# Kernel optimization log

Hardware: AMD Instinct MI355X
Metric: run time of the kernel (lower is better)

## Reference

```python
import jax, jax.numpy as jnp
import numpy as np

B, N, F_DIM = 64, 4096, 64
K_SLOTS, D, N_ITERS = 8, 64, 3
EPS = 1e-8
LN_EPS = 1e-5  # torch LayerNorm default


def layernorm(x, g, b):
    mu = jnp.mean(x, axis=-1, keepdims=True)
    var = jnp.mean(jnp.square(x - mu), axis=-1, keepdims=True)
    return (x - mu) * jax.lax.rsqrt(var + LN_EPS) * g + b


def gru_cell(x, h, w_ih, w_hh, b_ih, b_hh):
    # torch.nn.GRUCell semantics; weights are [3D, D] with gate order r, z, n
    gi = x @ w_ih.T + b_ih
    gh = h @ w_hh.T + b_hh
    i_r, i_z, i_n = jnp.split(gi, 3, axis=-1)
    h_r, h_z, h_n = jnp.split(gh, 3, axis=-1)
    r = jax.nn.sigmoid(i_r + h_r)
    z = jax.nn.sigmoid(i_z + h_z)
    n = jnp.tanh(i_n + r * h_n)
    return (1.0 - z) * n + z * h


def setup_inputs() -> dict:
    key = jax.random.key(0)
    ks = jax.random.split(key, 16)
    f32 = jnp.float32
    s = 0.05  # small init scale for weights
    return {
        "inputs": jax.random.normal(ks[0], (B, N, F_DIM), f32),
        "slots_noise": jax.random.normal(ks[1], (B, K_SLOTS, D), f32),
        "slots_mu": jax.random.normal(ks[2], (1, 1, D), f32) * s,
        "slots_log_sigma": jax.random.normal(ks[3], (1, 1, D), f32) * s,
        "Wq": jax.random.normal(ks[4], (D, D), f32) * s,
        "Wk": jax.random.normal(ks[5], (D, F_DIM), f32) * s,
        "Wv": jax.random.normal(ks[6], (D, F_DIM), f32) * s,
        "gru_w_ih": jax.random.normal(ks[7], (3 * D, D), f32) * s,
        "gru_w_hh": jax.random.normal(ks[8], (3 * D, D), f32) * s,
        "gru_b_ih": jnp.zeros((3 * D,), f32),
        "gru_b_hh": jnp.zeros((3 * D,), f32),
        "mlp_w1": jax.random.normal(ks[9], (2 * D, D), f32) * s,
        "mlp_b1": jnp.zeros((2 * D,), f32),
        "mlp_w2": jax.random.normal(ks[10], (D, 2 * D), f32) * s,
        "mlp_b2": jnp.zeros((D,), f32),
        "ln_in_g": jnp.ones((F_DIM,), f32), "ln_in_b": jnp.zeros((F_DIM,), f32),
        "ln_slots_g": jnp.ones((D,), f32), "ln_slots_b": jnp.zeros((D,), f32),
        "ln_mlp_g": jnp.ones((D,), f32), "ln_mlp_b": jnp.zeros((D,), f32),
    }


def reference(inputs, slots_noise, slots_mu, slots_log_sigma, Wq, Wk, Wv,
              gru_w_ih, gru_w_hh, gru_b_ih, gru_b_hh,
              mlp_w1, mlp_b1, mlp_w2, mlp_b2,
              ln_in_g, ln_in_b, ln_slots_g, ln_slots_b, ln_mlp_g, ln_mlp_b):
    x = layernorm(inputs, ln_in_g, ln_in_b)          # [B, N, F]
    k = jnp.einsum('bnf,df->bnd', x, Wk)             # [B, N, D]
    v = jnp.einsum('bnf,df->bnd', x, Wv)             # [B, N, D]

    slots = slots_mu + jnp.exp(slots_log_sigma) * slots_noise  # [B, K, D]
    scale = D ** -0.5

    for _ in range(N_ITERS):
        slots_prev = slots
        s_n = layernorm(slots, ln_slots_g, ln_slots_b)
        q = jnp.einsum('bkd,ed->bke', s_n, Wq)                  # [B, K, D]
        attn_logits = jnp.einsum('bnd,bkd->bnk', k, q) * scale  # [B, N, K]
        attn = jax.nn.softmax(attn_logits, axis=-1) + EPS       # softmax over slots
        attn = attn / jnp.sum(attn, axis=1, keepdims=True)      # renormalize over N
        updates = jnp.einsum('bnk,bnd->bkd', attn, v)           # [B, K, D]
        slots = gru_cell(updates.reshape(-1, D), slots_prev.reshape(-1, D),
                         gru_w_ih, gru_w_hh, gru_b_ih, gru_b_hh).reshape(B, K_SLOTS, D)
        h = layernorm(slots, ln_mlp_g, ln_mlp_b)
        h = jax.nn.relu(h @ mlp_w1.T + mlp_b1) @ mlp_w2.T + mlp_b2
        slots = slots + h
    return slots
```

## Files before the change

### kernel.cpp

```cpp
#include <hip/hip_runtime.h>
#include <math.h>

#define NN 4096
#define LN_EPS 1e-5f
#define EPS 1e-8f

typedef unsigned short ushortT;
typedef unsigned int uintT;
typedef __attribute__((ext_vector_type(8))) short short8;
typedef __attribute__((ext_vector_type(4))) float f32x4;
typedef __attribute__((ext_vector_type(2))) float f32x2;
typedef __attribute__((ext_vector_type(4))) unsigned short us4;

#define OFF_XN    0L
#define OFF_QU    8388608L
#define OFF_AP    8486912L
#define OFF_CP    9273344L
#define OFF_SLOTS 9285632L
#define OFF_WIHT  9383936L
#define OFF_WHHT  9396224L
#define OFF_W1T   9408512L
#define OFF_W2T   9416704L
#define OFF_WQT   9424896L
#define OFF_WVT   9428992L
#define OFF_CNT   9433088L
#define OFF_RDY   9433280L

__device__ __forceinline__ float wredsum(float v) {
#pragma unroll
  for (int off = 32; off > 0; off >>= 1) v += __shfl_xor(v, off);
  return v;
}

__device__ __forceinline__ ushortT f2bf(float f) {
  uintT b = __float_as_uint(f);
  b += 0x7fff + ((b >> 16) & 1);
  return (ushortT)(b >> 16);
}

__device__ __forceinline__ uintT pack2bf(float lo, float hi) {
  return (uintT)f2bf(lo) | ((uintT)f2bf(hi) << 16);
}

__device__ __forceinline__ void store2_coh(float* p, f32x2 v) {
  asm volatile("global_store_dwordx2 %0, %1, off sc0 sc1" :: "v"(p), "v"(v) : "memory");
}
__device__ __forceinline__ void store1f_coh(float* p, float v) {
  asm volatile("global_store_dword %0, %1, off sc0 sc1" :: "v"(p), "v"(v) : "memory");
}
__device__ __forceinline__ void store1u_coh(uintT* p, uintT v) {
  asm volatile("global_store_dword %0, %1, off sc0 sc1" :: "v"(p), "v"(v) : "memory");
}
__device__ __forceinline__ uintT load1u_coh(const uintT* p) {
  uintT r;
  asm volatile("global_load_dword %0, %1, off sc0 sc1\n\t"
               "s_waitcnt vmcnt(0)" : "=v"(r) : "v"(p) : "memory");
  return r;
}
__device__ __forceinline__ void drain_vm() {
  asm volatile("s_waitcnt vmcnt(0)" ::: "memory");
}

__global__ __launch_bounds__(256) void k_prep(
    const float* __restrict__ w_ih, const float* __restrict__ w_hh,
    const float* __restrict__ w1, const float* __restrict__ w2,
    const float* __restrict__ Wq, const float* __restrict__ Wv,
    float* __restrict__ wihT, float* __restrict__ whhT,
    float* __restrict__ w1T, float* __restrict__ w2T, float* __restrict__ wqT,
    float* __restrict__ wvT, uintT* __restrict__ cnt, uintT* __restrict__ ready)
{
  int idx = blockIdx.x * 256 + threadIdx.x;
  if (idx < 12288) {
    int j = idx >> 6, f = idx & 63;
    wihT[f * 192 + j] = w_ih[idx];
  } else if (idx < 24576) {
    int i = idx - 12288; int j = i >> 6, f = i & 63;
    whhT[f * 192 + j] = w_hh[i];
  } else if (idx < 32768) {
    int i = idx - 24576; int j = i >> 6, f = i & 63;
    w1T[f * 128 + j] = w1[i];
  } else if (idx < 40960) {
    int i = idx - 32768; int d = i >> 7, j = i & 127;
    w2T[j * 64 + d] = w2[i];
  } else if (idx < 45056) {
    int i = idx - 40960; int e = i >> 6, d = i & 63;
    wqT[d * 64 + e] = Wq[i];
  } else if (idx < 49152) {
    int i = idx - 45056; int d = i >> 6, f = i & 63;
    wvT[f * 64 + d] = Wv[i];
  } else if (idx < 49344) {
    cnt[idx - 49152] = 0u;
  } else if (idx < 49408) {
    ready[idx - 49344] = 0u;
  }
}

__global__ __launch_bounds__(256) void k_ln_init(
    const float* __restrict__ inp,
    const float* __restrict__ g, const float* __restrict__ bbv,
    ushortT* __restrict__ xnG,
    const float* __restrict__ noise, const float* __restrict__ smu,
    const float* __restrict__ slsig, const float* __restrict__ wqT,
    const float* __restrict__ Wk,
    const float* __restrict__ g_sl, const float* __restrict__ b_sl,
    float* __restrict__ slotsV, uintT* __restrict__ qU)
{
  __shared__ __align__(16) ushortT xnF[4096];
  const int tid = threadIdx.x;
  const int lane = tid & 63;
  const int wave = tid >> 6;

  if (blockIdx.x >= 4096) {
    const int bi = blockIdx.x - 4096;
    const int row = bi * 4 + wave;
    const int b = row >> 3, ks = row & 7;
    float* SI = (float*)&xnF[0];
    float* Sw = SI + (wave << 9);

    float s0 = fmaf(expf(slsig[lane]), noise[row * 64 + lane], smu[lane]);
    slotsV[row * 64 + lane] = s0;

    float mu = wredsum(s0) * (1.f / 64.f);
    float dx = s0 - mu;
    float var = wredsum(dx * dx) * (1.f / 64.f);
    float sn = dx * rsqrtf(var + LN_EPS) * g_sl[lane] + b_sl[lane];
    Sw[lane] = sn;
    float qe = 0.f;
#pragma unroll 16
    for (int d = 0; d < 64; ++d) qe = fmaf(Sw[d], wqT[d * 64 + lane], qe);
    Sw[64 + lane] = qe;
    float qp = 0.f;
#pragma unroll 16
    for (int e = 0; e < 64; ++e) qp = fmaf(Sw[64 + e], Wk[e * 64 + lane], qp);
    Sw[128 + lane] = qp * 0.125f;
    if (lane < 32) {
      const int kb = lane >> 4, lrow = (lane >> 2) & 3, j2 = lane & 3;
      const int fA = kb * 32 + lrow * 8 + 2 * j2;
      uintT u = pack2bf(Sw[128 + fA], Sw[128 + fA + 1]);
      qU[((b * 2 + kb) * 64 + lrow * 16 + ks) * 4 + j2] = u;
#pragma unroll
      for (int v = 0; v < 3; ++v)
        qU[v * 32768 + ((b * 2 + kb) * 64 + lrow * 16 + 8 + ks) * 4 + j2] = 0u;
    }
    return;
  }

  const int l15 = lane & 15, q = lane >> 4;
  const int tile = blockIdx.x;
  const int b = tile >> 6;
  const int c = tile & 63;
  const int n0 = c << 6;
  const float* rowbase = inp + (((long)b * NN + n0) << 6);
  const float4 g4 = *(const float4*)&g[l15 << 2];
  const float4 b4 = *(const float4*)&bbv[l15 << 2];

#pragma unroll
  for (int i = 0; i < 4; ++i) {
    const int row = (wave << 4) + (i << 2) + q;
    float4 x = *(const float4*)&rowbase[(row << 6) + (l15 << 2)];
    float s = x.x + x.y + x.z + x.w;
    s += __shfl_xor(s, 1); s += __shfl_xor(s, 2);
    s += __shfl_xor(s, 4); s += __shfl_xor(s, 8);
    const float mu = s * (1.f / 64.f);
    float4 dx = {x.x - mu, x.y - mu, x.z - mu, x.w - mu};
    float ss = dx.x * dx.x + dx.y * dx.y + dx.z * dx.z + dx.w * dx.w;
    ss += __shfl_xor(ss, 1); ss += __shfl_xor(ss, 2);
    ss += __shfl_xor(ss, 4); ss += __shfl_xor(ss, 8);
    const float rs = rsqrtf(ss * (1.f / 64.f) + LN_EPS);
    us4 p = {f2bf(dx.x * rs * g4.x + b4.x), f2bf(dx.y * rs * g4.y + b4.y),
             f2bf(dx.z * rs * g4.z + b4.z), f2bf(dx.w * rs * g4.w + b4.w)};
    *(us4*)&xnF[((((wave << 1) + (l15 >> 3)) << 6) + (((l15 & 7) >> 1) << 4)
                 + (row & 15)) * 8 + ((l15 & 1) << 2)] = p;
  }
  __syncthreads();

  ushortT* dst = xnG + ((long)(b * 64 + c) << 12);
  short8 v0 = *(const short8*)&xnF[tid << 4];
  short8 v1 = *(const short8*)&xnF[(tid << 4) + 8];
  *(short8*)&dst[tid << 4] = v0;
  *(short8*)&dst[(tid << 4) + 8] = v1;
}

__global__ __launch_bounds__(256, 2) void k_attn(
    const ushortT* __restrict__ xnG, uintT* __restrict__ qU,
    float* __restrict__ accPart, float* __restrict__ colPart,
    uintT* __restrict__ cnt, uintT* __restrict__ ready,
    float* __restrict__ slotsV,
    const float* __restrict__ wihT, const float* __restrict__ whhT,
    const float* __restrict__ w1T, const float* __restrict__ w2T,
    const float* __restrict__ wqT, const float* __restrict__ Wk,
    const float* __restrict__ wvT,
    const float* __restrict__ b_ih, const float* __restrict__ b_hh,
    const float* __restrict__ mb1, const float* __restrict__ mb2,
    const float* __restrict__ g_ml, const float* __restrict__ b_ml,
    const float* __restrict__ g_sl, const float* __restrict__ b_sl,
    float* __restrict__ dout)
{
  __shared__ __align__(16) ushortT XW[4][4096];
  __shared__ int lastFlag;
  const int tid = threadIdx.x;
  const int lane = tid & 63;
  const int wave = tid >> 6;
  const int l15 = lane & 15, q = lane >> 4;
  const int b = blockIdx.x >> 3;
  const int e = blockIdx.x & 7;

  ushortT* xT = &XW[wave][0];

  const ushortT* pc0 = xnG + ((long)(b * 64 + (e << 3) + wave) << 12);
  const ushortT* pc1 = pc0 + (4L << 12);

  short8 kA0[4][2], kA1[4][2];
#pragma unroll
  for (int mt = 0; mt < 4; ++mt)
#pragma unroll
    for (int kb = 0; kb < 2; ++kb) {
      kA0[mt][kb] = *(const short8*)&pc0[((mt * 2 + kb) * 64 + lane) << 3];
      kA1[mt][kb] = *(const short8*)&pc1[((mt * 2 + kb) * 64 + lane) << 3];
    }

  short8 vB0[4][2], vB1[4][2];
  {
    const int h = ((lane >> 5) << 2) | (((lane & 15) >> 3) << 1) | ((lane >> 4) & 1);
    const int jp = lane & 7;
    const int lpA = (((lane >> 4) & 1) << 3) + (((lane & 15) >> 3) << 4);
#pragma unroll
    for (int ch = 0; ch < 2; ++ch) {
#pragma unroll
      for (int mt = 0; mt < 4; ++mt)
#pragma unroll
        for (int kb = 0; kb < 2; ++kb) {
          const int fb = (kb * 4 + ((lane >> 5) << 1) + (mt >> 1)) << 9;
          const int lm = lpA + ((mt & 1) << 5);
          const short8 src8 = ch ? kA1[mt][kb] : kA0[mt][kb];
          const ushortT* src = (const ushortT*)&src8;
#pragma unroll
          for (int j = 0; j < 8; ++j)
            xT[fb + (((lm + j) ^ h) << 3) + jp] = src[j];
        }
#pragma unroll
      for (int nt = 0; nt < 4; ++nt)
#pragma unroll
        for (int ks = 0; ks < 2; ++ks) {
          const int frag = nt * 2 + ks;
          const int hr = ((nt & 1) << 2) | (((lane >> 4) & 1) << 1) | ((lane >> 3) & 1);
          short8 v = *(const short8*)&xT[(frag << 9) + ((lane ^ hr) << 3)];
          if (ch) vB1[nt][ks] = v; else vB0[nt][ks] = v;
        }
    }
  }

  for (int it = 0; it < 3; ++it) {
    if (it > 0) {
      if (tid == 0) {
        while (load1u_coh(&ready[b]) < (uintT)it) __builtin_amdgcn_s_sleep(2);
      }
      __syncthreads();
    }

    const uintT* qIt = qU + it * 32768;
    short8 qB[2];
#pragma unroll
    for (int kb = 0; kb < 2; ++kb)
      qB[kb] = *(const short8*)&qIt[((b * 2 + kb) * 64 + lane) * 4];

    f32x4 accP[4];
#pragma unroll
    for (int nt = 0; nt < 4; ++nt) accP[nt] = (f32x4){0.f, 0.f, 0.f, 0.f};
    float csum = 0.f;

#pragma unroll
    for (int ch = 0; ch < 2; ++ch) {
      f32x4 accL[4];
#pragma unroll
      for (int mt = 0; mt < 4; ++mt) {
        const short8 a0 = ch ? kA1[mt][0] : kA0[mt][0];
        const short8 a1 = ch ? kA1[mt][1] : kA0[mt][1];
        accL[mt] = (f32x4){0.f, 0.f, 0.f, 0.f};
        accL[mt] = __builtin_amdgcn_mfma_f32_16x16x32_bf16(a0, qB[0], accL[mt], 0, 0, 0);
        accL[mt] = __builtin_amdgcn_mfma_f32_16x16x32_bf16(a1, qB[1], accL[mt], 0, 0, 0);
      }

      ushortT* attnF = &XW[wave][0];
#pragma unroll
      for (int mt = 0; mt < 4; ++mt) {
        float av[4];
#pragma unroll
        for (int r = 0; r < 4; ++r) {
          float lv = accL[mt][r];
          float mx = lv;
          mx = fmaxf(mx, __shfl_xor(mx, 1));
          mx = fmaxf(mx, __shfl_xor(mx, 2));
          mx = fmaxf(mx, __shfl_xor(mx, 4));
          float ev = __expf(lv - mx);
          float sv = ev;
          sv += __shfl_xor(sv, 1); sv += __shfl_xor(sv, 2); sv += __shfl_xor(sv, 4);
          float a = ev * (1.f / sv) + EPS;
          av[r] = a;
          csum += a;
        }
        us4 p = {f2bf(av[0]), f2bf(av[1]), f2bf(av[2]), f2bf(av[3])};
        *(us4*)&attnF[((((mt >> 1) << 6) + (((mt & 1) * 2 + (q >> 1)) << 4)
                        + l15) << 3) + ((q & 1) << 2)] = p;
      }

      short8 pA0 = *(const short8*)&attnF[(0 * 64 + lane) << 3];
      short8 pA1 = *(const short8*)&attnF[(1 * 64 + lane) << 3];

#pragma unroll
      for (int nt = 0; nt < 4; ++nt) {
        const short8 v0 = ch ? vB1[nt][0] : vB0[nt][0];
        const short8 v1 = ch ? vB1[nt][1] : vB0[nt][1];
        accP[nt] = __builtin_amdgcn_mfma_f32_16x16x32_bf16(pA0, v0, accP[nt], 0, 0, 0);
        accP[nt] = __builtin_amdgcn_mfma_f32_16x16x32_bf16(pA1, v1, accP[nt], 0, 0, 0);
      }
    }

    csum += __shfl_xor(csum, 16);
    csum += __shfl_xor(csum, 32);

    float* accLw = (float*)&XW[wave][1024];
    float* colLw = (float*)&XW[wave][2048];
    if (q < 2) {
#pragma unroll
      for (int nt = 0; nt < 4; ++nt)
#pragma unroll
        for (int r = 0; r < 4; ++r)
          accLw[(q * 4 + r) * 64 + nt * 16 + l15] = accP[nt][r];
    }
    if (q == 0 && l15 < 8) colLw[l15] = csum;
    __syncthreads();

    float* apIt = accPart + ((long)(it * 64 + b) * 8 + e) * 512;
    float* cpIt = colPart + ((long)(it * 64 + b) * 8 + e) * 8;
    {
      const int o = tid * 2;
      f32x2 s;
#pragma unroll
      for (int r = 0; r < 2; ++r) {
        const int oo = o + r;
        s[r] = *((float*)&XW[0][1024] + oo) + *((float*)&XW[1][1024] + oo)
             + *((float*)&XW[2][1024] + oo) + *((float*)&XW[3][1024] + oo);
      }
      store2_coh(&apIt[o], s);
    }
    if (tid < 8) {
      float s = *((float*)&XW[0][2048] + tid) + *((float*)&XW[1][2048] + tid)
              + *((float*)&XW[2][2048] + tid) + *((float*)&XW[3][2048] + tid);
      store1f_coh(&cpIt[tid], s);
    }

    drain_vm();
    __syncthreads();
    if (tid == 0) lastFlag = (atomicAdd(&cnt[it * 64 + b], 1u) == 7u);
    __syncthreads();

    if (lastFlag) {
      const int ks0 = wave, ks1 = wave + 4;
      const int row0 = b * 8 + ks0, row1 = b * 8 + ks1;
      const float* apB = accPart + (long)(it * 64 + b) * 8 * 512;
      const float* cpB = colPart + (long)(it * 64 + b) * 8 * 8;
      const float* slIt = slotsV + it * 32768;

      float csv0 = 0.f, csv1 = 0.f, t0 = 0.f, t1 = 0.f;
#pragma unroll
      for (int ee = 0; ee < 8; ++ee) {
        csv0 += cpB[ee * 8 + ks0];
        csv1 += cpB[ee * 8 + ks1];
        t0 += apB[ee * 512 + ks0 * 64 + lane];
        t1 += apB[ee * 512 + ks1 * 64 + lane];
      }
      t0 /= csv0; t1 /= csv1;
      const float h0 = slIt[row0 * 64 + lane];
      const float h1 = slIt[row1 * 64 + lane];

      float* S = (float*)&XW[wave][0];

      S[256 + lane] = t0; S[320 + lane] = t1;
      float u0 = 0.f, u1 = 0.f;
#pragma unroll 4
      for (int f = 0; f < 64; ++f) {
        const float wv = wvT[f * 64 + lane];
        u0 = fmaf(S[256 + f], wv, u0);
        u1 = fmaf(S[320 + f], wv, u1);
      }

      S[lane] = u0; S[64 + lane] = u1; S[128 + lane] = h0; S[192 + lane] = h1;

      float gir0 = b_ih[lane], giz0 = b_ih[64 + lane], gin0 = b_ih[128 + lane];
      float ghr0 = b_hh[lane], ghz0 = b_hh[64 + lane], ghn0 = b_hh[128 + lane];
      float gir1 = gir0, giz1 = giz0, gin1 = gin0;
      float ghr1 = ghr0, ghz1 = ghz0, ghn1 = ghn0;
#pragma unroll 4
      for (int f = 0; f < 64; ++f) {
        const float wr = wihT[f * 192 + lane], wz = wihT[f * 192 + 64 + lane],
                    wn = wihT[f * 192 + 128 + lane];
        const float vr = whhT[f * 192 + lane], vz = whhT[f * 192 + 64 + lane],
                    vn = whhT[f * 192 + 128 + lane];
        const float a0 = S[f], a1 = S[64 + f], c0 = S[128 + f], c1 = S[192 + f];
        gir0 = fmaf(a0, wr, gir0); gir1 = fmaf(a1, wr, gir1);
        giz0 = fmaf(a0, wz, giz0); giz1 = fmaf(a1, wz, giz1);
        gin0 = fmaf(a0, wn, gin0); gin1 = fmaf(a1, wn, gin1);
        ghr0 = fmaf(c0, vr, ghr0); ghr1 = fmaf(c1, vr, ghr1);
        ghz0 = fmaf(c0, vz, ghz0); ghz1 = fmaf(c1, vz, ghz1);
        ghn0 = fmaf(c0, vn, ghn0); ghn1 = fmaf(c1, vn, ghn1);
      }
      const float r0 = 1.f / (1.f + expf(-(gir0 + ghr0)));
      const float z0 = 1.f / (1.f + expf(-(giz0 + ghz0)));
      const float n0 = tanhf(fmaf(r0, ghn0, gin0));
      const float hn0 = (1.f - z0) * n0 + z0 * h0;
      const float r1 = 1.f / (1.f + expf(-(gir1 + ghr1)));
      const float z1 = 1.f / (1.f + expf(-(giz1 + ghz1)));
      const float n1 = tanhf(fmaf(r1, ghn1, gin1));
      const float hn1 = (1.f - z1) * n1 + z1 * h1;

      float mu0 = wredsum(hn0) * (1.f / 64.f);
      float dx0 = hn0 - mu0;
      float va0 = wredsum(dx0 * dx0) * (1.f / 64.f);
      const float ln0 = dx0 * rsqrtf(va0 + LN_EPS) * g_ml[lane] + b_ml[lane];
      float mu1 = wredsum(hn1) * (1.f / 64.f);
      float dx1 = hn1 - mu1;
      float va1 = wredsum(dx1 * dx1) * (1.f / 64.f);
      const float ln1 = dx1 * rsqrtf(va1 + LN_EPS) * g_ml[lane] + b_ml[lane];
      S[256 + lane] = ln0; S[320 + lane] = ln1;

      float h1a0 = mb1[lane], h1b0 = mb1[64 + lane];
      float h1a1 = h1a0, h1b1 = h1b0;
#pragma unroll 4
      for (int f = 0; f < 64; ++f) {
        const float wa = w1T[f * 128 + lane], wb = w1T[f * 128 + 64 + lane];
        const float l0 = S[256 + f], l1 = S[320 + f];
        h1a0 = fmaf(l0, wa, h1a0); h1a1 = fmaf(l1, wa, h1a1);
        h1b0 = fmaf(l0, wb, h1b0); h1b1 = fmaf(l1, wb, h1b1);
      }
      h1a0 = fmaxf(h1a0, 0.f); h1b0 = fmaxf(h1b0, 0.f);
      h1a1 = fmaxf(h1a1, 0.f); h1b1 = fmaxf(h1b1, 0.f);
      S[lane] = h1a0; S[64 + lane] = h1b0;
      S[128 + lane] = h1a1; S[192 + lane] = h1b1;

      float o0 = mb2[lane], o1 = mb2[lane];
#pragma unroll 4
      for (int j = 0; j < 128; ++j) {
        const float w2v = w2T[j * 64 + lane];
        o0 = fmaf(S[j], w2v, o0);
        o1 = fmaf(S[128 + j], w2v, o1);
      }
      const float sn0 = hn0 + o0;
      const float sn1 = hn1 + o1;

      if (it == 2) {
        dout[row0 * 64 + lane] = sn0;
        dout[row1 * 64 + lane] = sn1;
      } else {
        float* slN = slotsV + (it + 1) * 32768;
        store1f_coh(&slN[row0 * 64 + lane], sn0);
        store1f_coh(&slN[row1 * 64 + lane], sn1);

        float m20 = wredsum(sn0) * (1.f / 64.f);
        float d20 = sn0 - m20;
        float v20 = wredsum(d20 * d20) * (1.f / 64.f);
        const float sq0 = d20 * rsqrtf(v20 + LN_EPS) * g_sl[lane] + b_sl[lane];
        float m21 = wredsum(sn1) * (1.f / 64.f);
        float d21 = sn1 - m21;
        float v21 = wredsum(d21 * d21) * (1.f / 64.f);
        const float sq1 = d21 * rsqrtf(v21 + LN_EPS) * g_sl[lane] + b_sl[lane];
        S[256 + lane] = sq0; S[320 + lane] = sq1;
        float qe0 = 0.f, qe1 = 0.f;
#pragma unroll 8
        for (int d = 0; d < 64; ++d) {
          const float wq = wqT[d * 64 + lane];
          qe0 = fmaf(S[256 + d], wq, qe0);
          qe1 = fmaf(S[320 + d], wq, qe1);
        }
        S[256 + lane] = qe0; S[320 + lane] = qe1;
        float qp0 = 0.f, qp1 = 0.f;
#pragma unroll 8
        for (int e2 = 0; e2 < 64; ++e2) {
          const float wk = Wk[e2 * 64 + lane];
          qp0 = fmaf(S[256 + e2], wk, qp0);
          qp1 = fmaf(S[320 + e2], wk, qp1);
        }
        S[384 + lane] = qp0 * 0.125f;
        S[448 + lane] = qp1 * 0.125f;
        {
          uintT* qN = qU + (it + 1) * 32768;
          const int rr = lane >> 5, L5 = lane & 31;
          const int kb = L5 >> 4, lrow = (L5 >> 2) & 3, j2 = L5 & 3;
          const int fA = kb * 32 + lrow * 8 + 2 * j2;
          const int ksr = rr ? ks1 : ks0;
          uintT u = pack2bf(S[384 + rr * 64 + fA], S[384 + rr * 64 + fA + 1]);
          store1u_coh(&qN[((b * 2 + kb) * 64 + lrow * 16 + ksr) * 4 + j2], u);
        }
        drain_vm();
        __syncthreads();
        if (tid == 0) atomicAdd(&ready[b], 1u);
      }
    }
  }
}

extern "C" void kernel_launch(void* const* d_in, const int* in_sizes, int n_in,
                              void* d_out, int out_size, void* d_ws, size_t ws_size,
                              hipStream_t stream) {
  const float* inp   = (const float*)d_in[0];
  const float* noise = (const float*)d_in[1];
  const float* smu   = (const float*)d_in[2];
  const float* slsig = (const float*)d_in[3];
  const float* Wq    = (const float*)d_in[4];
  const float* Wk    = (const float*)d_in[5];
  const float* Wv    = (const float*)d_in[6];
  const float* w_ih  = (const float*)d_in[7];
  const float* w_hh  = (const float*)d_in[8];
  const float* b_ih  = (const float*)d_in[9];
  const float* b_hh  = (const float*)d_in[10];
  const float* w1    = (const float*)d_in[11];
  const float* b1    = (const float*)d_in[12];
  const float* w2    = (const float*)d_in[13];
  const float* b2    = (const float*)d_in[14];
  const float* g_in  = (const float*)d_in[15];
  const float* bi_in = (const float*)d_in[16];
  const float* g_sl  = (const float*)d_in[17];
  const float* bi_sl = (const float*)d_in[18];
  const float* g_ml  = (const float*)d_in[19];
  const float* bi_ml = (const float*)d_in[20];

  float* ws      = (float*)d_ws;
  ushortT* xnG   = (ushortT*)(ws + OFF_XN);
  uintT* qU      = (uintT*)(ws + OFF_QU);
  float* ap      = ws + OFF_AP;
  float* cp      = ws + OFF_CP;
  float* sl      = ws + OFF_SLOTS;
  float* wihT    = ws + OFF_WIHT;
  float* whhT    = ws + OFF_WHHT;
  float* w1T     = ws + OFF_W1T;
  float* w2T     = ws + OFF_W2T;
  float* wqT     = ws + OFF_WQT;
  float* wvT     = ws + OFF_WVT;
  uintT* cnt     = (uintT*)(ws + OFF_CNT);
  uintT* rdy     = (uintT*)(ws + OFF_RDY);

  k_prep<<<194, 256, 0, stream>>>(w_ih, w_hh, w1, w2, Wq, Wv,
                                  wihT, whhT, w1T, w2T, wqT, wvT, cnt, rdy);
  k_ln_init<<<4224, 256, 0, stream>>>(inp, g_in, bi_in, xnG,
                                      noise, smu, slsig, wqT, Wk, g_sl, bi_sl,
                                      sl, qU);
  k_attn<<<512, 256, 0, stream>>>(xnG, qU, ap, cp, cnt, rdy, sl,
                                  wihT, whhT, w1T, w2T, wqT, Wk, wvT,
                                  b_ih, b_hh, b1, b2, g_ml, bi_ml, g_sl, bi_sl,
                                  (float*)d_out);
}
```

Measured before the change: 268.4 us.

## Fuse input LayerNorm into attention kernel and drop bf16 staging buffer

Input LayerNorm and bf16 conversion now run inside the persistent attention kernel, reading the fp32 inputs directly instead of a 16 MB bf16 intermediate written by a separate kernel. Slot init and q-projection move into the weight-prep kernel, which removes one launch. The V-operand transpose is recomputed through LDS on every iteration instead of being held in registers, which lowers register pressure but adds LDS traffic inside the loop. The trade-off is that the attention kernel reads 64 MB of fp32 instead of 32 MB of bf16, in return for skipping a write and a read of the intermediate.

```diff
diff --git a/kernel.cpp b/kernel.cpp
--- a/kernel.cpp
+++ b/kernel.cpp
@@ -12,19 +12,18 @@
 typedef __attribute__((ext_vector_type(2))) float f32x2;
 typedef __attribute__((ext_vector_type(4))) unsigned short us4;
 
-#define OFF_XN    0L
-#define OFF_QU    8388608L
-#define OFF_AP    8486912L
-#define OFF_CP    9273344L
-#define OFF_SLOTS 9285632L
-#define OFF_WIHT  9383936L
-#define OFF_WHHT  9396224L
-#define OFF_W1T   9408512L
-#define OFF_W2T   9416704L
-#define OFF_WQT   9424896L
-#define OFF_WVT   9428992L
-#define OFF_CNT   9433088L
-#define OFF_RDY   9433280L
+#define OFF_QU    0L
+#define OFF_AP    98304L
+#define OFF_CP    884736L
+#define OFF_SLOTS 897024L
+#define OFF_WIHT  995328L
+#define OFF_WHHT  1007616L
+#define OFF_W1T   1019904L
+#define OFF_W2T   1028096L
+#define OFF_WQT   1036288L
+#define OFF_WVT   1040384L
+#define OFF_CNT   1044480L
+#define OFF_RDY   1044672L
 
 __device__ __forceinline__ float wredsum(float v) {
 #pragma unroll
@@ -60,16 +59,61 @@
 __device__ __forceinline__ void drain_vm() {
   asm volatile("s_waitcnt vmcnt(0)" ::: "memory");
 }
+__device__ __forceinline__ void wait_lds() {
+  asm volatile("s_waitcnt lgkmcnt(0)" ::: "memory");
+}
 
 __global__ __launch_bounds__(256) void k_prep(
     const float* __restrict__ w_ih, const float* __restrict__ w_hh,
     const float* __restrict__ w1, const float* __restrict__ w2,
     const float* __restrict__ Wq, const float* __restrict__ Wv,
+    const float* __restrict__ Wk,
+    const float* __restrict__ noise, const float* __restrict__ smu,
+    const float* __restrict__ slsig,
+    const float* __restrict__ g_sl, const float* __restrict__ b_sl,
     float* __restrict__ wihT, float* __restrict__ whhT,
     float* __restrict__ w1T, float* __restrict__ w2T, float* __restrict__ wqT,
-    float* __restrict__ wvT, uintT* __restrict__ cnt, uintT* __restrict__ ready)
+    float* __restrict__ wvT, float* __restrict__ slotsV, uintT* __restrict__ qU,
+    uintT* __restrict__ cnt, uintT* __restrict__ ready)
 {
-  int idx = blockIdx.x * 256 + threadIdx.x;
+  const int tid = threadIdx.x;
+  if (blockIdx.x >= 194) {
+    __shared__ float SI[4][192];
+    const int lane = tid & 63, wave = tid >> 6;
+    const int bi = blockIdx.x - 194;
+    const int row = bi * 4 + wave;
+    const int b = row >> 3, ks = row & 7;
+    float* Sw = SI[wave];
+
+    float s0 = fmaf(expf(slsig[lane]), noise[row * 64 + lane], smu[lane]);
+    slotsV[row * 64 + lane] = s0;
+
+    float mu = wredsum(s0) * (1.f / 64.f);
+    float dx = s0 - mu;
+    float var = wredsum(dx * dx) * (1.f / 64.f);
+    float sn = dx * rsqrtf(var + LN_EPS) * g_sl[lane] + b_sl[lane];
+    Sw[lane] = sn;
+    float qe = 0.f;
+#pragma unroll 16
+    for (int d = 0; d < 64; ++d) qe = fmaf(Sw[d], Wq[lane * 64 + d], qe);
+    Sw[64 + lane] = qe;
+    float qp = 0.f;
+#pragma unroll 16
+    for (int e = 0; e < 64; ++e) qp = fmaf(Sw[64 + e], Wk[e * 64 + lane], qp);
+    Sw[128 + lane] = qp * 0.125f;
+    if (lane < 32) {
+      const int kb = lane >> 4, lrow = (lane >> 2) & 3, j2 = lane & 3;
+      const int fA = kb * 32 + lrow * 8 + 2 * j2;
+      uintT u = pack2bf(Sw[128 + fA], Sw[128 + fA + 1]);
+      qU[((b * 2 + kb) * 64 + lrow * 16 + ks) * 4 + j2] = u;
+#pragma unroll
+      for (int v = 0; v < 3; ++v)
+        qU[v * 32768 + ((b * 2 + kb) * 64 + lrow * 16 + 8 + ks) * 4 + j2] = 0u;
+    }
+    return;
+  }
+
+  int idx = blockIdx.x * 256 + tid;
   if (idx < 12288) {
     int j = idx >> 6, f = idx & 63;
     wihT[f * 192 + j] = w_ih[idx];
@@ -95,94 +139,10 @@
   }
 }
 
-__global__ __launch_bounds__(256) void k_ln_init(
+__global__ __launch_bounds__(256, 2) void k_attn(
     const float* __restrict__ inp,
-    const float* __restrict__ g, const float* __restrict__ bbv,
-    ushortT* __restrict__ xnG,
-    const float* __restrict__ noise, const float* __restrict__ smu,
-    const float* __restrict__ slsig, const float* __restrict__ wqT,
-    const float* __restrict__ Wk,
-    const float* __restrict__ g_sl, const float* __restrict__ b_sl,
-    float* __restrict__ slotsV, uintT* __restrict__ qU)
-{
-  __shared__ __align__(16) ushortT xnF[4096];
-  const int tid = threadIdx.x;
-  const int lane = tid & 63;
-  const int wave = tid >> 6;
-
-  if (blockIdx.x >= 4096) {
-    const int bi = blockIdx.x - 4096;
-    const int row = bi * 4 + wave;
-    const int b = row >> 3, ks = row & 7;
-    float* SI = (float*)&xnF[0];
-    float* Sw = SI + (wave << 9);
-
-    float s0 = fmaf(expf(slsig[lane]), noise[row * 64 + lane], smu[lane]);
-    slotsV[row * 64 + lane] = s0;
-
-    float mu = wredsum(s0) * (1.f / 64.f);
-    float dx = s0 - mu;
-    float var = wredsum(dx * dx) * (1.f / 64.f);
-    float sn = dx * rsqrtf(var + LN_EPS) * g_sl[lane] + b_sl[lane];
-    Sw[lane] = sn;
-    float qe = 0.f;
-#pragma unroll 16
-    for (int d = 0; d < 64; ++d) qe = fmaf(Sw[d], wqT[d * 64 + lane], qe);
-    Sw[64 + lane] = qe;
-    float qp = 0.f;
-#pragma unroll 16
-    for (int e = 0; e < 64; ++e) qp = fmaf(Sw[64 + e], Wk[e * 64 + lane], qp);
-    Sw[128 + lane] = qp * 0.125f;
-    if (lane < 32) {
-      const int kb = lane >> 4, lrow = (lane >> 2) & 3, j2 = lane & 3;
-      const int fA = kb * 32 + lrow * 8 + 2 * j2;
-      uintT u = pack2bf(Sw[128 + fA], Sw[128 + fA + 1]);
-      qU[((b * 2 + kb) * 64 + lrow * 16 + ks) * 4 + j2] = u;
-#pragma unroll
-      for (int v = 0; v < 3; ++v)
-        qU[v * 32768 + ((b * 2 + kb) * 64 + lrow * 16 + 8 + ks) * 4 + j2] = 0u;
-    }
-    return;
-  }
-
-  const int l15 = lane & 15, q = lane >> 4;
-  const int tile = blockIdx.x;
-  const int b = tile >> 6;
-  const int c = tile & 63;
-  const int n0 = c << 6;
-  const float* rowbase = inp + (((long)b * NN + n0) << 6);
-  const float4 g4 = *(const float4*)&g[l15 << 2];
-  const float4 b4 = *(const float4*)&bbv[l15 << 2];
-
-#pragma unroll
-  for (int i = 0; i < 4; ++i) {
-    const int row = (wave << 4) + (i << 2) + q;
-    float4 x = *(const float4*)&rowbase[(row << 6) + (l15 << 2)];
-    float s = x.x + x.y + x.z + x.w;
-    s += __shfl_xor(s, 1); s += __shfl_xor(s, 2);
-    s += __shfl_xor(s, 4); s += __shfl_xor(s, 8);
-    const float mu = s * (1.f / 64.f);
-    float4 dx = {x.x - mu, x.y - mu, x.z - mu, x.w - mu};
-    float ss = dx.x * dx.x + dx.y * dx.y + dx.z * dx.z + dx.w * dx.w;
-    ss += __shfl_xor(ss, 1); ss += __shfl_xor(ss, 2);
-    ss += __shfl_xor(ss, 4); ss += __shfl_xor(ss, 8);
-    const float rs = rsqrtf(ss * (1.f / 64.f) + LN_EPS);
-    us4 p = {f2bf(dx.x * rs * g4.x + b4.x), f2bf(dx.y * rs * g4.y + b4.y),
-             f2bf(dx.z * rs * g4.z + b4.z), f2bf(dx.w * rs * g4.w + b4.w)};
-    *(us4*)&xnF[((((wave << 1) + (l15 >> 3)) << 6) + (((l15 & 7) >> 1) << 4)
-                 + (row & 15)) * 8 + ((l15 & 1) << 2)] = p;
-  }
-  __syncthreads();
-
-  ushortT* dst = xnG + ((long)(b * 64 + c) << 12);
-  short8 v0 = *(const short8*)&xnF[tid << 4];
-  short8 v1 = *(const short8*)&xnF[(tid << 4) + 8];
-  *(short8*)&dst[tid << 4] = v0;
-  *(short8*)&dst[(tid << 4) + 8] = v1;
-}
-
-__global__ __launch_bounds__(256, 2) void k_attn(
-    const ushortT* __restrict__ xnG, uintT* __restrict__ qU,
+    const float* __restrict__ g_in, const float* __restrict__ b_in,
+    uintT* __restrict__ qU,
     float* __restrict__ accPart, float* __restrict__ colPart,
     uintT* __restrict__ cnt, uintT* __restrict__ ready,
     float* __restrict__ slotsV,
@@ -207,46 +167,42 @@
 
   ushortT* xT = &XW[wave][0];
 
-  const ushortT* pc0 = xnG + ((long)(b * 64 + (e << 3) + wave) << 12);
-  const ushortT* pc1 = pc0 + (4L << 12);
-
   short8 kA0[4][2], kA1[4][2];
-#pragma unroll
-  for (int mt = 0; mt < 4; ++mt)
-#pragma unroll
-    for (int kb = 0; kb < 2; ++kb) {
-      kA0[mt][kb] = *(const short8*)&pc0[((mt * 2 + kb) * 64 + lane) << 3];
-      kA1[mt][kb] = *(const short8*)&pc1[((mt * 2 + kb) * 64 + lane) << 3];
-    }
-
-  short8 vB0[4][2], vB1[4][2];
   {
-    const int h = ((lane >> 5) << 2) | (((lane & 15) >> 3) << 1) | ((lane >> 4) & 1);
-    const int jp = lane & 7;
-    const int lpA = (((lane >> 4) & 1) << 3) + (((lane & 15) >> 3) << 4);
+    const float4 g4 = *(const float4*)&g_in[l15 << 2];
+    const float4 b4 = *(const float4*)&b_in[l15 << 2];
 #pragma unroll
     for (int ch = 0; ch < 2; ++ch) {
+      const int chunk = (e << 3) + (ch << 2) + wave;
+      const float* rowbase = inp + (((long)b * NN + (chunk << 6)) << 6);
+#pragma unroll
+      for (int pass = 0; pass < 16; ++pass) {
+        const int row = (pass << 2) + q;
+        float4 x = *(const float4*)&rowbase[(row << 6) + (l15 << 2)];
+        float s = x.x + x.y + x.z + x.w;
+        s += __shfl_xor(s, 1); s += __shfl_xor(s, 2);
+        s += __shfl_xor(s, 4); s += __shfl_xor(s, 8);
+        const float mu = s * (1.f / 64.f);
+        float4 dx = {x.x - mu, x.y - mu, x.z - mu, x.w - mu};
+        float ss = dx.x * dx.x + dx.y * dx.y + dx.z * dx.z + dx.w * dx.w;
+        ss += __shfl_xor(ss, 1); ss += __shfl_xor(ss, 2);
+        ss += __shfl_xor(ss, 4); ss += __shfl_xor(ss, 8);
+        const float rs = rsqrtf(ss * (1.f / 64.f) + LN_EPS);
+        us4 p = {f2bf(dx.x * rs * g4.x + b4.x), f2bf(dx.y * rs * g4.y + b4.y),
+                 f2bf(dx.z * rs * g4.z + b4.z), f2bf(dx.w * rs * g4.w + b4.w)};
+        *(us4*)&xT[((((row >> 4) * 2 + (l15 >> 3)) << 6)
+                    + (((l15 & 7) >> 1) << 4) + (row & 15)) * 8
+                   + ((l15 & 1) << 2)] = p;
+      }
+      wait_lds();
 #pragma unroll
       for (int mt = 0; mt < 4; ++mt)
 #pragma unroll
         for (int kb = 0; kb < 2; ++kb) {
-          const int fb = (kb * 4 + ((lane >> 5) << 1) + (mt >> 1)) << 9;
-          const int lm = lpA + ((mt & 1) << 5);
-          const short8 src8 = ch ? kA1[mt][kb] : kA0[mt][kb];
-          const ushortT* src = (const ushortT*)&src8;
-#pragma unroll
-          for (int j = 0; j < 8; ++j)
-            xT[fb + (((lm + j) ^ h) << 3) + jp] = src[j];
+          short8 v = *(const short8*)&xT[((mt * 2 + kb) * 64 + lane) << 3];
+          if (ch) kA1[mt][kb] = v; else kA0[mt][kb] = v;
         }
-#pragma unroll
-      for (int nt = 0; nt < 4; ++nt)
-#pragma unroll
-        for (int ks = 0; ks < 2; ++ks) {
-          const int frag = nt * 2 + ks;
-          const int hr = ((nt & 1) << 2) | (((lane >> 4) & 1) << 1) | ((lane >> 3) & 1);
-          short8 v = *(const short8*)&xT[(frag << 9) + ((lane ^ hr) << 3)];
-          if (ch) vB1[nt][ks] = v; else vB0[nt][ks] = v;
-        }
+      wait_lds();
     }
   }
 
@@ -280,6 +236,33 @@
         accL[mt] = __builtin_amdgcn_mfma_f32_16x16x32_bf16(a0, qB[0], accL[mt], 0, 0, 0);
         accL[mt] = __builtin_amdgcn_mfma_f32_16x16x32_bf16(a1, qB[1], accL[mt], 0, 0, 0);
       }
+
+      {
+        const int h = ((lane >> 5) << 2) | (((lane & 15) >> 3) << 1) | ((lane >> 4) & 1);
+        const int jp = lane & 7;
+        const int lpA = (((lane >> 4) & 1) << 3) + (((lane & 15) >> 3) << 4);
+#pragma unroll
+        for (int mt = 0; mt < 4; ++mt)
+#pragma unroll
+          for (int kb = 0; kb < 2; ++kb) {
+            const int fb = (kb * 4 + ((lane >> 5) << 1) + (mt >> 1)) << 9;
+            const int lm = lpA + ((mt & 1) << 5);
+            const short8 src8 = ch ? kA1[mt][kb] : kA0[mt][kb];
+            const ushortT* src = (const ushortT*)&src8;
+#pragma unroll
+            for (int j = 0; j < 8; ++j)
+              xT[fb + (((lm + j) ^ h) << 3) + jp] = src[j];
+          }
+      }
+      short8 vB[4][2];
+#pragma unroll
+      for (int nt = 0; nt < 4; ++nt)
+#pragma unroll
+        for (int ks = 0; ks < 2; ++ks) {
+          const int frag = nt * 2 + ks;
+          const int hr = ((nt & 1) << 2) | (((lane >> 4) & 1) << 1) | ((lane >> 3) & 1);
+          vB[nt][ks] = *(const short8*)&xT[(frag << 9) + ((lane ^ hr) << 3)];
+        }
 
       ushortT* attnF = &XW[wave][0];
 #pragma unroll
@@ -309,10 +292,8 @@
 
 #pragma unroll
       for (int nt = 0; nt < 4; ++nt) {
-        const short8 v0 = ch ? vB1[nt][0] : vB0[nt][0];
-        const short8 v1 = ch ? vB1[nt][1] : vB0[nt][1];
-        accP[nt] = __builtin_amdgcn_mfma_f32_16x16x32_bf16(pA0, v0, accP[nt], 0, 0, 0);
-        accP[nt] = __builtin_amdgcn_mfma_f32_16x16x32_bf16(pA1, v1, accP[nt], 0, 0, 0);
+        accP[nt] = __builtin_amdgcn_mfma_f32_16x16x32_bf16(pA0, vB[nt][0], accP[nt], 0, 0, 0);
+        accP[nt] = __builtin_amdgcn_mfma_f32_16x16x32_bf16(pA1, vB[nt][1], accP[nt], 0, 0, 0);
       }
     }
 
@@ -525,7 +506,6 @@
   const float* bi_ml = (const float*)d_in[20];
 
   float* ws      = (float*)d_ws;
-  ushortT* xnG   = (ushortT*)(ws + OFF_XN);
   uintT* qU      = (uintT*)(ws + OFF_QU);
   float* ap      = ws + OFF_AP;
   float* cp      = ws + OFF_CP;
@@ -539,12 +519,11 @@
   uintT* cnt     = (uintT*)(ws + OFF_CNT);
   uintT* rdy     = (uintT*)(ws + OFF_RDY);
 
-  k_prep<<<194, 256, 0, stream>>>(w_ih, w_hh, w1, w2, Wq, Wv,
-                                  wihT, whhT, w1T, w2T, wqT, wvT, cnt, rdy);
-  k_ln_init<<<4224, 256, 0, stream>>>(inp, g_in, bi_in, xnG,
-                                      noise, smu, slsig, wqT, Wk, g_sl, bi_sl,
-                                      sl, qU);
-  k_attn<<<512, 256, 0, stream>>>(xnG, qU, ap, cp, cnt, rdy, sl,
+  k_prep<<<322, 256, 0, stream>>>(w_ih, w_hh, w1, w2, Wq, Wv, Wk,
+                                  noise, smu, slsig, g_sl, bi_sl,
+                                  wihT, whhT, w1T, w2T, wqT, wvT,
+                                  sl, qU, cnt, rdy);
+  k_attn<<<512, 256, 0, stream>>>(inp, g_in, bi_in, qU, ap, cp, cnt, rdy, sl,
                                   wihT, whhT, w1T, w2T, wqT, Wk, wvT,
                                   b_ih, b_hh, b1, b2, g_ml, bi_ml, g_sl, bi_sl,
                                   (float*)d_out);
```

Result: faster. 244.8 us (-8.8%).
